# Optimization experiments

Hardware: AMD Instinct MI355X
Metric: run time of the kernel (lower is better)

## Reference

```python
import jax, jax.numpy as jnp
import numpy as np

N, B, T, C = 1024, 4, 12, 64
D, H, K, E = 64, 2, 3, 16384  # out_dim, gat heads, num_kernel, edges per kernel
NEG_SLOPE_ATTN = 0.2   # DGL GATConv default
NEG_SLOPE_ACT = 0.01   # nn.LeakyReLU default


def setup_inputs() -> dict:
    key = jax.random.key(0)
    ks = jax.random.split(key, 12)
    input_feature = jax.random.normal(ks[0], (B, N, T, C), dtype=jnp.float32)
    # edge lists per kernel, with self loops appended (dgl.add_self_loop)
    loops = jnp.broadcast_to(jnp.arange(N, dtype=jnp.int32), (K, N))
    src_idx = jnp.concatenate(
        [jax.random.randint(ks[1], (K, E), 0, N, dtype=jnp.int32), loops], axis=1)
    dst_idx = jnp.concatenate(
        [jax.random.randint(ks[2], (K, E), 0, N, dtype=jnp.int32), loops], axis=1)
    # GATConv params per kernel: fc (no bias), attn_l/attn_r, output bias
    fc_w = jax.random.normal(ks[3], (K, C, H * D), dtype=jnp.float32) * 0.1
    attn_l = jax.random.normal(ks[4], (K, H, D), dtype=jnp.float32) * 0.1
    attn_r = jax.random.normal(ks[5], (K, H, D), dtype=jnp.float32) * 0.1
    gat_bias = jax.random.normal(ks[6], (K, H * D), dtype=jnp.float32) * 0.02
    # per-kernel merge weight, init std 0.05 as in init_weight()
    weight = jax.random.normal(ks[7], (K,), dtype=jnp.float32) * 0.05
    # merge MLP: Linear(H*D -> D)
    merge_w = jax.random.normal(ks[8], (H * D, D), dtype=jnp.float32) * 0.05
    merge_b = jax.random.normal(ks[9], (D,), dtype=jnp.float32) * 0.02
    return {"input_feature": input_feature, "fc_w": fc_w, "attn_l": attn_l,
            "attn_r": attn_r, "gat_bias": gat_bias, "weight": weight,
            "merge_w": merge_w, "merge_b": merge_b,
            "src_idx": src_idx, "dst_idx": dst_idx}


def _gat_conv(x, fc_w, attn_l, attn_r, bias, src, dst):
    """DGL GATConv on feature x: [N,B,T,C] -> [N,B,T,H,D]."""
    feat = jnp.einsum('nbtc,ce->nbte', x, fc_w).reshape(N, B, T, H, D)
    el = jnp.einsum('nbthd,hd->nbth', feat, attn_l)  # [N,B,T,H]
    er = jnp.einsum('nbthd,hd->nbth', feat, attn_r)
    e = jax.nn.leaky_relu(el[src] + er[dst], NEG_SLOPE_ATTN)  # [Etot,B,T,H]
    # segment softmax over destination neighborhoods (self loops guarantee >=1 edge)
    emax = jax.ops.segment_max(e, dst, num_segments=N)
    a = jnp.exp(e - emax[dst])
    denom = jax.ops.segment_sum(a, dst, num_segments=N)
    alpha = a / denom[dst]
    msg = alpha[..., None] * feat[src]  # [Etot,B,T,H,D]
    rst = jax.ops.segment_sum(msg, dst, num_segments=N)
    return rst + bias.reshape(H, D)


def reference(input_feature, fc_w, attn_l, attn_r, gat_bias, weight,
              merge_w, merge_b, src_idx, dst_idx):
    x = jnp.transpose(input_feature, (1, 0, 2, 3))  # [N,B,T,C]
    result = jnp.zeros((N, B, T, H, D), dtype=x.dtype)
    for i in range(K):  # small fixed set of dilated kernels
        result = result + weight[i] * _gat_conv(
            x, fc_w[i], attn_l[i], attn_r[i], gat_bias[i], src_idx[i], dst_idx[i])
    merged = result.reshape(N, B, T, H * D) @ merge_w + merge_b  # [N,B,T,D]
    out = jax.nn.leaky_relu(merged, NEG_SLOPE_ACT) + x  # residual = Identity (C==D)
    return jnp.transpose(out, (1, 0, 2, 3))  # [B,N,T,D]
```

## Files before the change

### kernel.cpp

```cpp
#include <hip/hip_runtime.h>

#define NN   1024
#define TT   12
#define CC   64
#define DD   64
#define HH   2
#define KK   3
#define ETOT 17408
#define BT   48
#define BTH  96
#define HD   128
#define NODES (KK * NN + 1)
#define PADN  (KK * NN)
#define CSR_CAP (KK * ETOT + 12 * NN)
#define LOG2E 1.44269504f
#define MT   128
#define NBLK (NN * BT / MT)
#define EDGE_BLOCKS ((KK * ETOT + 255) / 256)
#define FEAT_BLOCKS (KK * NBLK)
#define BIG_BLOCKS (EDGE_BLOCKS + FEAT_BLOCKS + NN)
#define RUNCAP 208

typedef __attribute__((ext_vector_type(8))) short s8v;
typedef __attribute__((ext_vector_type(4))) float f4v;

__device__ __forceinline__ float bf_lo(unsigned int u) {
    return __uint_as_float(u << 16);
}
__device__ __forceinline__ float bf_hi(unsigned int u) {
    return __uint_as_float(u & 0xFFFF0000u);
}
__device__ __forceinline__ unsigned short f2bf(float f) {
    unsigned int u = __float_as_uint(f);
    u += 0x7FFFu + ((u >> 16) & 1u);
    return (unsigned short)(u >> 16);
}
__device__ __forceinline__ unsigned int pack2(float a, float b) {
    return (unsigned int)f2bf(a) | ((unsigned int)f2bf(b) << 16);
}
__device__ __forceinline__ float rlf(float v, int lane) {
    return __int_as_float(__builtin_amdgcn_readlane(__float_as_int(v), lane));
}

__global__ __launch_bounds__(256) void aux_kernel(
    const int* __restrict__ dst_idx, int* __restrict__ counts,
    const float* __restrict__ fc_w, const float* __restrict__ attn_l,
    const float* __restrict__ attn_r, float* __restrict__ alc, float* __restrict__ arc,
    uint2* __restrict__ featp, float* __restrict__ elp)
{
    int bid = blockIdx.x;
    int t = threadIdx.x;
    if (bid < EDGE_BLOCKS) {
        int tid = bid * 256 + t;
        if (tid < KK * ETOT) {
            int k = tid / ETOT;
            atomicAdd(&counts[k * NN + dst_idx[tid]], 1);
        }
    } else {
        for (int item = t; item < KK * HH * CC; item += 256) {
            int kh = item >> 6, c = item & 63;
            int k = kh >> 1, h = kh & 1;
            float sl = 0.f, sr = 0.f;
            #pragma unroll
            for (int dd = 0; dd < 64; ++dd) {
                float wv = fc_w[k * CC * HD + c * HD + h * 64 + dd];
                sl = fmaf(wv, attn_l[k * HD + h * 64 + dd], sl);
                sr = fmaf(wv, attn_r[k * HD + h * 64 + dd], sr);
            }
            alc[item] = sl * LOG2E;
            arc[item] = sr * LOG2E;
        }
        for (int item = t; item < 24 * 64; item += 256)
            featp[((size_t)(item >> 6) * NODES + PADN) * 64 + (item & 63)] = make_uint2(0u, 0u);
        for (int item = t; item < 24 * 4; item += 256)
            elp[((size_t)(item >> 2) * NODES + PADN) * 4 + (item & 3)] = -1e30f;
    }
}

__global__ __launch_bounds__(1024) void scan_kernel(
    const int* __restrict__ counts,
    int4* __restrict__ segs, int* __restrict__ cursor, int* __restrict__ csr_comb)
{
    int n = threadIdx.x;
    int c0 = counts[n], c1 = counts[NN + n], c2 = counts[2 * NN + n];
    int p0 = (c0 + 3) & ~3, p1 = (c1 + 3) & ~3, p2 = (c2 + 3) & ~3;
    int tot = p0 + p1 + p2;
    __shared__ int buf[NN];
    buf[n] = tot;
    __syncthreads();
    for (int off = 1; off < NN; off <<= 1) {
        int v = (n >= off) ? buf[n - off] : 0;
        __syncthreads();
        buf[n] += v;
        __syncthreads();
    }
    int excl = buf[n] - tot;
    int4 sg;
    sg.x = excl; sg.y = excl + p0; sg.z = excl + p0 + p1; sg.w = excl + tot;
    segs[n] = sg;
    cursor[n] = sg.x;
    cursor[NN + n] = sg.y;
    cursor[2 * NN + n] = sg.z;
    for (int j = sg.x + c0; j < sg.y; ++j) csr_comb[j] = PADN;
    for (int j = sg.y + c1; j < sg.z; ++j) csr_comb[j] = PADN;
    for (int j = sg.z + c2; j < sg.w; ++j) csr_comb[j] = PADN;
}

__global__ __launch_bounds__(256) void big_kernel(
    const int* __restrict__ src_idx, const int* __restrict__ dst_idx,
    int* __restrict__ cursor, int* __restrict__ csr_comb,
    const float* __restrict__ x, const float* __restrict__ fc_w,
    uint2* __restrict__ featp,
    const float* __restrict__ alc, const float* __restrict__ arc,
    float* __restrict__ elp, float* __restrict__ er)
{
    __shared__ __align__(16) char smem[32768];
    int bid = blockIdx.x;
    int t = threadIdx.x;

    if (bid < EDGE_BLOCKS) {
        int tid = bid * 256 + t;
        if (tid < KK * ETOT) {
            int k = tid / ETOT;
            int pos = atomicAdd(&cursor[k * NN + dst_idx[tid]], 1);
            csr_comb[pos] = k * NN + src_idx[tid];
        }
        return;
    }
    if (bid < EDGE_BLOCKS + FEAT_BLOCKS) {
        int kb = bid - EDGE_BLOCKS;
        int k  = kb / NBLK;
        int m0 = (kb - k * NBLK) * MT;
        int w  = t >> 6, l = t & 63;
        unsigned short* As = (unsigned short*)smem;
        unsigned short* Ws = (unsigned short*)(smem + 16384);

        #pragma unroll
        for (int rep = 0; rep < 4; ++rep) {
            int gid = t + 256 * rep;
            int row = gid >> 3, g = gid & 7;
            int m = m0 + row;
            int n = m / BT, bt = m - n * BT;
            int b = bt / TT, tt2 = bt - b * TT;
            const float* xr = &x[(((size_t)b * NN + n) * TT + tt2) * CC + g * 8];
            float4 v0 = *(const float4*)xr;
            float4 v1 = *(const float4*)(xr + 4);
            uint4 pk = { pack2(v0.x, v0.y), pack2(v0.z, v0.w),
                         pack2(v1.x, v1.y), pack2(v1.z, v1.w) };
            *(uint4*)((char*)As + row * 128 + ((g ^ (row & 7)) << 4)) = pk;
        }
        #pragma unroll
        for (int rep = 0; rep < 4; ++rep) {
            int gid = t + 256 * rep;
            int e = gid & 127, g = gid >> 7;
            float v[8];
            #pragma unroll
            for (int jj = 0; jj < 8; ++jj)
                v[jj] = fc_w[(size_t)k * CC * HD + (g * 8 + jj) * HD + e];
            uint4 pk = { pack2(v[0], v[1]), pack2(v[2], v[3]),
                         pack2(v[4], v[5]), pack2(v[6], v[7]) };
            *(uint4*)((char*)Ws + e * 128 + ((g ^ (e & 7)) << 4)) = pk;
        }
        __syncthreads();

        int Mw = (w & 1) * 64;
        int Nw = (w >> 1) * 64;
        int rsel = l & 15, ksel = l >> 4;

        f4v acc[4][4];
        #pragma unroll
        for (int mi = 0; mi < 4; ++mi)
            #pragma unroll
            for (int nf = 0; nf < 4; ++nf)
                acc[mi][nf] = (f4v){0.f, 0.f, 0.f, 0.f};

        s8v af[4][2], bf[4][2];
        #pragma unroll
        for (int mi = 0; mi < 4; ++mi)
            #pragma unroll
            for (int ks = 0; ks < 2; ++ks) {
                int row = Mw + mi * 16 + rsel;
                int g = ks * 4 + ksel;
                af[mi][ks] = *(const s8v*)((const char*)As + row * 128 + ((g ^ (row & 7)) << 4));
            }
        #pragma unroll
        for (int nf = 0; nf < 4; ++nf)
            #pragma unroll
            for (int ks = 0; ks < 2; ++ks) {
                int e = Nw + nf * 16 + rsel;
                int g = ks * 4 + ksel;
                bf[nf][ks] = *(const s8v*)((const char*)Ws + e * 128 + ((g ^ (e & 7)) << 4));
            }

        #pragma unroll
        for (int mi = 0; mi < 4; ++mi)
            #pragma unroll
            for (int nf = 0; nf < 4; ++nf) {
                acc[mi][nf] = __builtin_amdgcn_mfma_f32_16x16x32_bf16(
                    af[mi][0], bf[nf][0], acc[mi][nf], 0, 0, 0);
                acc[mi][nf] = __builtin_amdgcn_mfma_f32_16x16x32_bf16(
                    af[mi][1], bf[nf][1], acc[mi][nf], 0, 0, 0);
            }

        int i0 = (l >> 4) * 4;
        #pragma unroll
        for (int mi = 0; mi < 4; ++mi) {
            int m = m0 + Mw + mi * 16 + i0;
            int n = m / BT, bt = m - n * BT;
            #pragma unroll
            for (int nf = 0; nf < 4; ++nf) {
                int e = Nw + nf * 16 + (l & 15);
                int h = e >> 6, d = e & 63;
                int s = (bt >> 2) * 2 + h;
                uint2 o = { pack2(acc[mi][nf][0], acc[mi][nf][1]),
                            pack2(acc[mi][nf][2], acc[mi][nf][3]) };
                featp[((size_t)s * NODES + k * NN + n) * 64 + d] = o;
            }
        }
        return;
    }

    {
        int n = bid - (EDGE_BLOCKS + FEAT_BLOCKS);
        float* x_lds = (float*)smem;
        float* cl    = (float*)(smem + 12288);
        float* cr    = (float*)(smem + 12288 + 1536);

        for (int i = t; i < BT * CC; i += 256) {
            int bt = i >> 6, c = i & 63;
            int b = bt / TT, tt = bt - b * TT;
            x_lds[i] = x[(((size_t)b * NN + n) * TT + tt) * CC + c];
        }
        for (int i = t; i < KK * HH * CC; i += 256) { cl[i] = alc[i]; cr[i] = arc[i]; }
        __syncthreads();

        if (t < BTH) {
            int hh = t / BT, bt = t - hh * BT;
            #pragma unroll
            for (int k = 0; k < KK; ++k) {
                const float* alp = &cl[(k * HH + hh) * CC];
                const float* arp = &cr[(k * HH + hh) * CC];
                float sl = 0.f, sr = 0.f;
                #pragma unroll
                for (int cc = 0; cc < CC; ++cc) {
                    int c = (cc + bt) & 63;
                    float xv = x_lds[bt * CC + c];
                    sl = fmaf(xv, alp[c], sl);
                    sr = fmaf(xv, arp[c], sr);
                }
                int s = (bt >> 2) * 2 + hh;
                elp[((size_t)s * NODES + k * NN + n) * 4 + (bt & 3)] = sl;
                er[((size_t)(k * NN + n)) * BTH + t] = sr;
            }
        }
    }
}

#define EDGE_FMA8(F, A)                                        \
    r0 = fmaf((A).x, bf_lo((F).x), r0);                        \
    r1 = fmaf((A).y, bf_hi((F).x), r1);                        \
    r2 = fmaf((A).z, bf_lo((F).y), r2);                        \
    r3 = fmaf((A).w, bf_hi((F).y), r3);

#define PHASE1(JB, JE, KIDX, SC4) {                                            \
    int jb = (JB), je = (JE);                                                  \
    float erv = er[((size_t)((KIDX) * NN + n)) * BTH + h * BT + btg4 * 4 + bt];\
    float ss = 0.f;                                                            \
    for (int j0 = jb; j0 < je; j0 += 16) {                                     \
        int jj = j0 + joff;                                                    \
        float a = 0.f;                                                         \
        if (jj < je) {                                                         \
            int idx = csr_comb[jj];                                            \
            float ev = ep[idx * 4 + bt] + erv;                                 \
            ev = fmaxf(ev, ev * 0.2f);                                         \
            a = __builtin_amdgcn_exp2f(ev);                                    \
            alds[w][jj - base0][bt] = a;                                       \
        }                                                                      \
        ss += a;                                                               \
    }                                                                          \
    _Pragma("unroll")                                                          \
    for (int off = 4; off < 64; off <<= 1) ss += __shfl_xor(ss, off, 64);      \
    float wk_ = weight[KIDX];                                                  \
    SC4 = make_float4(wk_ * __builtin_amdgcn_rcpf(rlf(ss, 0)),                 \
                      wk_ * __builtin_amdgcn_rcpf(rlf(ss, 1)),                 \
                      wk_ * __builtin_amdgcn_rcpf(rlf(ss, 2)),                 \
                      wk_ * __builtin_amdgcn_rcpf(rlf(ss, 3))); }

#define PHASE2(JB, JE, SC4) {                                                  \
    int jb = __builtin_amdgcn_readfirstlane(JB);                               \
    int je = __builtin_amdgcn_readfirstlane(JE);                               \
    float r0 = 0.f, r1 = 0.f, r2 = 0.f, r3 = 0.f;                              \
    int jj = jb;                                                               \
    for (; jj + 8 <= je; jj += 8) {                                            \
        int4 ia = *(const int4*)&csr_comb[jj];                                 \
        int4 ib = *(const int4*)&csr_comb[jj + 4];                             \
        int i0 = __builtin_amdgcn_readfirstlane(ia.x);                         \
        int i1 = __builtin_amdgcn_readfirstlane(ia.y);                         \
        int i2 = __builtin_amdgcn_readfirstlane(ia.z);                         \
        int i3 = __builtin_amdgcn_readfirstlane(ia.w);                         \
        int i4 = __builtin_amdgcn_readfirstlane(ib.x);                         \
        int i5 = __builtin_amdgcn_readfirstlane(ib.y);                         \
        int i6 = __builtin_amdgcn_readfirstlane(ib.z);                         \
        int i7 = __builtin_amdgcn_readfirstlane(ib.w);                         \
        uint2 f0 = fb[(size_t)i0 * 64];                                        \
        uint2 f1 = fb[(size_t)i1 * 64];                                        \
        uint2 f2 = fb[(size_t)i2 * 64];                                        \
        uint2 f3 = fb[(size_t)i3 * 64];                                        \
        uint2 f4 = fb[(size_t)i4 * 64];                                        \
        uint2 f5 = fb[(size_t)i5 * 64];                                        \
        uint2 f6 = fb[(size_t)i6 * 64];                                        \
        uint2 f7 = fb[(size_t)i7 * 64];                                        \
        float4 A0 = *(const float4*)&alds[w][jj - base0 + 0][0];               \
        float4 A1 = *(const float4*)&alds[w][jj - base0 + 1][0];               \
        float4 A2 = *(const float4*)&alds[w][jj - base0 + 2][0];               \
        float4 A3 = *(const float4*)&alds[w][jj - base0 + 3][0];               \
        float4 A4 = *(const float4*)&alds[w][jj - base0 + 4][0];               \
        float4 A5 = *(const float4*)&alds[w][jj - base0 + 5][0];               \
        float4 A6 = *(const float4*)&alds[w][jj - base0 + 6][0];               \
        float4 A7 = *(const float4*)&alds[w][jj - base0 + 7][0];               \
        EDGE_FMA8(f0, A0); EDGE_FMA8(f1, A1);                                  \
        EDGE_FMA8(f2, A2); EDGE_FMA8(f3, A3);                                  \
        EDGE_FMA8(f4, A4); EDGE_FMA8(f5, A5);                                  \
        EDGE_FMA8(f6, A6); EDGE_FMA8(f7, A7);                                  \
    }                                                                          \
    if (jj < je) {                                                             \
        int4 ia = *(const int4*)&csr_comb[jj];                                 \
        int i0 = __builtin_amdgcn_readfirstlane(ia.x);                         \
        int i1 = __builtin_amdgcn_readfirstlane(ia.y);                         \
        int i2 = __builtin_amdgcn_readfirstlane(ia.z);                         \
        int i3 = __builtin_amdgcn_readfirstlane(ia.w);                         \
        uint2 f0 = fb[(size_t)i0 * 64];                                        \
        uint2 f1 = fb[(size_t)i1 * 64];                                        \
        uint2 f2 = fb[(size_t)i2 * 64];                                        \
        uint2 f3 = fb[(size_t)i3 * 64];                                        \
        float4 A0 = *(const float4*)&alds[w][jj - base0 + 0][0];               \
        float4 A1 = *(const float4*)&alds[w][jj - base0 + 1][0];               \
        float4 A2 = *(const float4*)&alds[w][jj - base0 + 2][0];               \
        float4 A3 = *(const float4*)&alds[w][jj - base0 + 3][0];               \
        EDGE_FMA8(f0, A0); EDGE_FMA8(f1, A1);                                  \
        EDGE_FMA8(f2, A2); EDGE_FMA8(f3, A3);                                  \
    }                                                                          \
    acc0 = fmaf(r0, (SC4).x, acc0); acc1 = fmaf(r1, (SC4).y, acc1);            \
    acc2 = fmaf(r2, (SC4).z, acc2); acc3 = fmaf(r3, (SC4).w, acc3); }

__global__ __launch_bounds__(256) void agg_kernel(
    const uint2* __restrict__ featp,
    const float* __restrict__ elp,
    const float* __restrict__ er,
    const int4* __restrict__ segs, const int* __restrict__ csr_comb,
    const float* __restrict__ gat_bias, const float* __restrict__ weight,
    unsigned short* __restrict__ gatb)
{
    int j = ((int)blockIdx.x >> 3) + 768 * ((int)blockIdx.x & 7);
    int s = j >> 8;
    int g = j & 255;
    int w = threadIdx.x >> 6;
    int l = threadIdx.x & 63;
    int n = g * 4 + w;
    int btg4 = s >> 1, h = s & 1;
    int e = h * 64 + l;

    __shared__ __align__(16) float alds[4][RUNCAP][4];

    const uint2* fb = featp + (size_t)s * NODES * 64 + l;
    const float* ep = elp + (size_t)s * NODES * 4;
    int4 sg = segs[n];
    int base0 = __builtin_amdgcn_readfirstlane(sg.x);

    int joff = l >> 2, bt = l & 3;
    float4 sc0, sc1, sc2;
    PHASE1(sg.x, sg.y, 0, sc0)
    PHASE1(sg.y, sg.z, 1, sc1)
    PHASE1(sg.z, sg.w, 2, sc2)

    float acc0 = 0.f, acc1 = 0.f, acc2 = 0.f, acc3 = 0.f;
    PHASE2(sg.x, sg.y, sc0)
    PHASE2(sg.y, sg.z, sc1)
    PHASE2(sg.z, sg.w, sc2)

    float wb = weight[0] * gat_bias[e] + weight[1] * gat_bias[HD + e]
             + weight[2] * gat_bias[2 * HD + e];
    acc0 += wb; acc1 += wb; acc2 += wb; acc3 += wb;

    size_t row = (size_t)n * BT + btg4 * 4;
    gatb[(row + 0) * HD + e] = f2bf(acc0);
    gatb[(row + 1) * HD + e] = f2bf(acc1);
    gatb[(row + 2) * HD + e] = f2bf(acc2);
    gatb[(row + 3) * HD + e] = f2bf(acc3);
}
#undef EDGE_FMA8
#undef PHASE1
#undef PHASE2

__global__ __launch_bounds__(256) void merge_mfma_kernel(
    const unsigned short* __restrict__ gatb,
    const float* __restrict__ merge_w, const float* __restrict__ merge_b,
    const float* __restrict__ x, float* __restrict__ out)
{
    int m0 = blockIdx.x * 128;
    int t = threadIdx.x, w = t >> 6, l = t & 63;

    __shared__ __align__(16) unsigned short As[128 * 128];
    __shared__ __align__(16) unsigned short Bs[64 * 128];

    #pragma unroll
    for (int rep = 0; rep < 8; ++rep) {
        int gid = t + 256 * rep;
        int row = gid >> 4, gg = gid & 15;
        uint4 v = *(const uint4*)((const char*)gatb + ((size_t)(m0 + row)) * 256 + gg * 16);
        *(uint4*)((char*)As + row * 256 + ((gg ^ (row & 15)) << 4)) = v;
    }
    #pragma unroll
    for (int rep = 0; rep < 4; ++rep) {
        int gid = t + 256 * rep;
        int col = gid >> 4, gg = gid & 15;
        float v[8];
        #pragma unroll
        for (int jj = 0; jj < 8; ++jj)
            v[jj] = merge_w[(gg * 8 + jj) * DD + col];
        uint4 pk = { pack2(v[0], v[1]), pack2(v[2], v[3]),
                     pack2(v[4], v[5]), pack2(v[6], v[7]) };
        *(uint4*)((char*)Bs + col * 256 + ((gg ^ (col & 15)) << 4)) = pk;
    }
    __syncthreads();

    int Mw = (w & 1) * 64, Nw = (w >> 1) * 32;
    int rsel = l & 15, ksel = l >> 4;

    f4v acc[4][2];
    #pragma unroll
    for (int mi = 0; mi < 4; ++mi)
        #pragma unroll
        for (int nf = 0; nf < 2; ++nf)
            acc[mi][nf] = (f4v){0.f, 0.f, 0.f, 0.f};

    s8v af[4][4], bfr[2][4];
    #pragma unroll
    for (int mi = 0; mi < 4; ++mi)
        #pragma unroll
        for (int ks = 0; ks < 4; ++ks) {
            int row = Mw + mi * 16 + rsel;
            int g2 = ks * 4 + ksel;
            af[mi][ks] = *(const s8v*)((const char*)As + row * 256 + ((g2 ^ (row & 15)) << 4));
        }
    #pragma unroll
    for (int nf = 0; nf < 2; ++nf)
        #pragma unroll
        for (int ks = 0; ks < 4; ++ks) {
            int col = Nw + nf * 16 + rsel;
            int g2 = ks * 4 + ksel;
            bfr[nf][ks] = *(const s8v*)((const char*)Bs + col * 256 + ((g2 ^ (col & 15)) << 4));
        }

    #pragma unroll
    for (int mi = 0; mi < 4; ++mi)
        #pragma unroll
        for (int nf = 0; nf < 2; ++nf)
            #pragma unroll
            for (int ks = 0; ks < 4; ++ks)
                acc[mi][nf] = __builtin_amdgcn_mfma_f32_16x16x32_bf16(
                    af[mi][ks], bfr[nf][ks], acc[mi][nf], 0, 0, 0);

    int i0 = (l >> 4) * 4;
    #pragma unroll
    for (int mi = 0; mi < 4; ++mi) {
        int m = m0 + Mw + mi * 16 + i0;
        int n = m / BT, btb = m - n * BT;
        int b = btb / TT, t0 = btb - b * TT;
        #pragma unroll
        for (int nf = 0; nf < 2; ++nf) {
            int dd = Nw + nf * 16 + (l & 15);
            float mb = merge_b[dd];
            #pragma unroll
            for (int reg = 0; reg < 4; ++reg) {
                float mg = acc[mi][nf][reg] + mb;
                mg = mg > 0.f ? mg : mg * 0.01f;
                size_t oidx = (((size_t)b * NN + n) * TT + t0 + reg) * DD + dd;
                out[oidx] = mg + x[oidx];
            }
        }
    }
}

extern "C" void kernel_launch(void* const* d_in, const int* in_sizes, int n_in,
                              void* d_out, int out_size, void* d_ws, size_t ws_size,
                              hipStream_t stream)
{
    const float* x        = (const float*)d_in[0];
    const float* fc_w     = (const float*)d_in[1];
    const float* attn_l   = (const float*)d_in[2];
    const float* attn_r   = (const float*)d_in[3];
    const float* gat_bias = (const float*)d_in[4];
    const float* weight   = (const float*)d_in[5];
    const float* merge_w  = (const float*)d_in[6];
    const float* merge_b  = (const float*)d_in[7];
    const int*   src_idx  = (const int*)d_in[8];
    const int*   dst_idx  = (const int*)d_in[9];
    float*       out      = (float*)d_out;

    char* p = (char*)d_ws;
    auto carve = [&](size_t bytes) { char* r = p; p += (bytes + 15) & ~size_t(15); return r; };
    uint2* featp   = (uint2*)carve(sizeof(uint2) * (size_t)24 * NODES * 64);
    unsigned short* gatb = (unsigned short*)carve(sizeof(unsigned short) * (size_t)NN * BT * HD);
    float* elp     = (float*)carve(sizeof(float) * (size_t)24 * NODES * 4);
    float* er      = (float*)carve(sizeof(float) * (size_t)KK * NN * BTH);
    float* alc     = (float*)carve(sizeof(float) * KK * HH * CC);
    float* arc     = (float*)carve(sizeof(float) * KK * HH * CC);
    int*   counts  = (int*)carve(sizeof(int) * KK * NN);
    int*   cursor  = (int*)carve(sizeof(int) * KK * NN);
    int4*  segs    = (int4*)carve(sizeof(int4) * NN);
    int*   csr_comb= (int*)carve(sizeof(int) * (CSR_CAP + 80));

    hipMemsetAsync(counts, 0, sizeof(int) * KK * NN, stream);

    aux_kernel<<<EDGE_BLOCKS + 1, 256, 0, stream>>>(
        dst_idx, counts, fc_w, attn_l, attn_r, alc, arc, featp, elp);

    scan_kernel<<<1, 1024, 0, stream>>>(counts, segs, cursor, csr_comb);

    big_kernel<<<BIG_BLOCKS, 256, 0, stream>>>(
        src_idx, dst_idx, cursor, csr_comb, x, fc_w, featp, alc, arc, elp, er);

    agg_kernel<<<24 * 256, 256, 0, stream>>>(
        featp, elp, er, segs, csr_comb, gat_bias, weight, gatb);

    merge_mfma_kernel<<<NN * BT / 128, 256, 0, stream>>>(gatb, merge_w, merge_b, x, out);
}
```

Measured before the change: 145.4 us.

## Widen feature slices to 8 bt per lane and interleave softmax/aggregate phases

Changes the packed feature layout from 24 slices of 4 bt values (uint2) to 12 slices of 8 bt values (uint4). The MFMA epilogue now pairs lanes with a shuffle so each writer stores one 16-byte chunk. The aggregation kernel processes 8 bt per lane, which halves the block count and the number of index loads and gathers per edge. It also runs each kernel's softmax phase right before its aggregation instead of all three first, so the LDS alpha buffer can be shorter (RUNCAP 144). The trade-offs are more registers per thread, fewer resident blocks, and a smaller per-segment cap on the LDS run buffer.

Measured after the change: 134.3 us. -7.6%, faster.

```diff
diff --git a/kernel.cpp b/kernel.cpp
--- a/kernel.cpp
+++ b/kernel.cpp
@@ -19,7 +19,8 @@
 #define EDGE_BLOCKS ((KK * ETOT + 255) / 256)
 #define FEAT_BLOCKS (KK * NBLK)
 #define BIG_BLOCKS (EDGE_BLOCKS + FEAT_BLOCKS + NN)
-#define RUNCAP 208
+#define NSL  12
+#define RUNCAP 144
 
 typedef __attribute__((ext_vector_type(8))) short s8v;
 typedef __attribute__((ext_vector_type(4))) float f4v;
@@ -46,7 +47,7 @@
     const int* __restrict__ dst_idx, int* __restrict__ counts,
     const float* __restrict__ fc_w, const float* __restrict__ attn_l,
     const float* __restrict__ attn_r, float* __restrict__ alc, float* __restrict__ arc,
-    uint2* __restrict__ featp, float* __restrict__ elp)
+    uint4* __restrict__ featp, float* __restrict__ elp)
 {
     int bid = blockIdx.x;
     int t = threadIdx.x;
@@ -70,10 +71,11 @@
             alc[item] = sl * LOG2E;
             arc[item] = sr * LOG2E;
         }
-        for (int item = t; item < 24 * 64; item += 256)
-            featp[((size_t)(item >> 6) * NODES + PADN) * 64 + (item & 63)] = make_uint2(0u, 0u);
-        for (int item = t; item < 24 * 4; item += 256)
-            elp[((size_t)(item >> 2) * NODES + PADN) * 4 + (item & 3)] = -1e30f;
+        for (int item = t; item < NSL * 64; item += 256)
+            featp[((size_t)(item >> 6) * NODES + PADN) * 64 + (item & 63)] =
+                make_uint4(0u, 0u, 0u, 0u);
+        for (int item = t; item < NSL * 8; item += 256)
+            elp[((size_t)(item >> 3) * NODES + PADN) * 8 + (item & 7)] = -1e30f;
     }
 }
 
@@ -110,7 +112,7 @@
     const int* __restrict__ src_idx, const int* __restrict__ dst_idx,
     int* __restrict__ cursor, int* __restrict__ csr_comb,
     const float* __restrict__ x, const float* __restrict__ fc_w,
-    uint2* __restrict__ featp,
+    uint4* __restrict__ featp,
     const float* __restrict__ alc, const float* __restrict__ arc,
     float* __restrict__ elp, float* __restrict__ er)
 {
@@ -203,18 +205,24 @@
             }
 
         int i0 = (l >> 4) * 4;
+        bool writer = ((l >> 4) & 1) == 0;
         #pragma unroll
         for (int mi = 0; mi < 4; ++mi) {
             int m = m0 + Mw + mi * 16 + i0;
             int n = m / BT, bt = m - n * BT;
             #pragma unroll
             for (int nf = 0; nf < 4; ++nf) {
-                int e = Nw + nf * 16 + (l & 15);
-                int h = e >> 6, d = e & 63;
-                int s = (bt >> 2) * 2 + h;
                 uint2 o = { pack2(acc[mi][nf][0], acc[mi][nf][1]),
                             pack2(acc[mi][nf][2], acc[mi][nf][3]) };
-                featp[((size_t)s * NODES + k * NN + n) * 64 + d] = o;
+                unsigned int px = (unsigned int)__shfl_xor((int)o.x, 16, 64);
+                unsigned int py = (unsigned int)__shfl_xor((int)o.y, 16, 64);
+                if (writer) {
+                    int e = Nw + nf * 16 + (l & 15);
+                    int h = e >> 6, d = e & 63;
+                    int s = ((bt >> 3) << 1) + h;
+                    featp[((size_t)s * NODES + k * NN + n) * 64 + d] =
+                        make_uint4(o.x, o.y, px, py);
+                }
             }
         }
         return;
@@ -248,147 +256,136 @@
                     sl = fmaf(xv, alp[c], sl);
                     sr = fmaf(xv, arp[c], sr);
                 }
-                int s = (bt >> 2) * 2 + hh;
-                elp[((size_t)s * NODES + k * NN + n) * 4 + (bt & 3)] = sl;
+                int s = ((bt >> 3) << 1) + hh;
+                elp[((size_t)s * NODES + k * NN + n) * 8 + (bt & 7)] = sl;
                 er[((size_t)(k * NN + n)) * BTH + t] = sr;
             }
         }
     }
 }
 
-#define EDGE_FMA8(F, A)                                        \
-    r0 = fmaf((A).x, bf_lo((F).x), r0);                        \
-    r1 = fmaf((A).y, bf_hi((F).x), r1);                        \
-    r2 = fmaf((A).z, bf_lo((F).y), r2);                        \
-    r3 = fmaf((A).w, bf_hi((F).y), r3);
-
-#define PHASE1(JB, JE, KIDX, SC4) {                                            \
+#define EFMA(F, LO, HI)                                        \
+    r0 = fmaf((LO).x, bf_lo((F).x), r0);                       \
+    r1 = fmaf((LO).y, bf_hi((F).x), r1);                       \
+    r2 = fmaf((LO).z, bf_lo((F).y), r2);                       \
+    r3 = fmaf((LO).w, bf_hi((F).y), r3);                       \
+    r4 = fmaf((HI).x, bf_lo((F).z), r4);                       \
+    r5 = fmaf((HI).y, bf_hi((F).z), r5);                       \
+    r6 = fmaf((HI).z, bf_lo((F).w), r6);                       \
+    r7 = fmaf((HI).w, bf_hi((F).w), r7);
+
+#define PHASE1(JB, JE, KIDX, SCLO, SCHI) {                                     \
     int jb = (JB), je = (JE);                                                  \
-    float erv = er[((size_t)((KIDX) * NN + n)) * BTH + h * BT + btg4 * 4 + bt];\
+    float erv = er[((size_t)((KIDX) * NN + n)) * BTH + h * BT + btg8 * 8 + btq];\
     float ss = 0.f;                                                            \
-    for (int j0 = jb; j0 < je; j0 += 16) {                                     \
+    for (int j0 = jb; j0 < je; j0 += 8) {                                      \
         int jj = j0 + joff;                                                    \
         float a = 0.f;                                                         \
         if (jj < je) {                                                         \
             int idx = csr_comb[jj];                                            \
-            float ev = ep[idx * 4 + bt] + erv;                                 \
+            float ev = elp[(size_t)sbase8 + (size_t)idx * 8 + btq] + erv;      \
             ev = fmaxf(ev, ev * 0.2f);                                         \
             a = __builtin_amdgcn_exp2f(ev);                                    \
-            alds[w][jj - base0][bt] = a;                                       \
+            alds[w][jj - base0][btq] = a;                                      \
         }                                                                      \
         ss += a;                                                               \
     }                                                                          \
-    _Pragma("unroll")                                                          \
-    for (int off = 4; off < 64; off <<= 1) ss += __shfl_xor(ss, off, 64);      \
+    ss += __shfl_xor(ss, 8, 64);                                               \
+    ss += __shfl_xor(ss, 16, 64);                                              \
+    ss += __shfl_xor(ss, 32, 64);                                              \
     float wk_ = weight[KIDX];                                                  \
-    SC4 = make_float4(wk_ * __builtin_amdgcn_rcpf(rlf(ss, 0)),                 \
-                      wk_ * __builtin_amdgcn_rcpf(rlf(ss, 1)),                 \
-                      wk_ * __builtin_amdgcn_rcpf(rlf(ss, 2)),                 \
-                      wk_ * __builtin_amdgcn_rcpf(rlf(ss, 3))); }
-
-#define PHASE2(JB, JE, SC4) {                                                  \
+    SCLO = make_float4(wk_ * __builtin_amdgcn_rcpf(rlf(ss, 0)),                \
+                       wk_ * __builtin_amdgcn_rcpf(rlf(ss, 1)),                \
+                       wk_ * __builtin_amdgcn_rcpf(rlf(ss, 2)),                \
+                       wk_ * __builtin_amdgcn_rcpf(rlf(ss, 3)));               \
+    SCHI = make_float4(wk_ * __builtin_amdgcn_rcpf(rlf(ss, 4)),                \
+                       wk_ * __builtin_amdgcn_rcpf(rlf(ss, 5)),                \
+                       wk_ * __builtin_amdgcn_rcpf(rlf(ss, 6)),                \
+                       wk_ * __builtin_amdgcn_rcpf(rlf(ss, 7))); }
+
+#define PHASE2(JB, JE, SCLO, SCHI) {                                           \
     int jb = __builtin_amdgcn_readfirstlane(JB);                               \
     int je = __builtin_amdgcn_readfirstlane(JE);                               \
-    float r0 = 0.f, r1 = 0.f, r2 = 0.f, r3 = 0.f;                              \
-    int jj = jb;                                                               \
-    for (; jj + 8 <= je; jj += 8) {                                            \
-        int4 ia = *(const int4*)&csr_comb[jj];                                 \
-        int4 ib = *(const int4*)&csr_comb[jj + 4];                             \
-        int i0 = __builtin_amdgcn_readfirstlane(ia.x);                         \
-        int i1 = __builtin_amdgcn_readfirstlane(ia.y);                         \
-        int i2 = __builtin_amdgcn_readfirstlane(ia.z);                         \
-        int i3 = __builtin_amdgcn_readfirstlane(ia.w);                         \
-        int i4 = __builtin_amdgcn_readfirstlane(ib.x);                         \
-        int i5 = __builtin_amdgcn_readfirstlane(ib.y);                         \
-        int i6 = __builtin_amdgcn_readfirstlane(ib.z);                         \
-        int i7 = __builtin_amdgcn_readfirstlane(ib.w);                         \
-        uint2 f0 = fb[(size_t)i0 * 64];                                        \
-        uint2 f1 = fb[(size_t)i1 * 64];                                        \
-        uint2 f2 = fb[(size_t)i2 * 64];                                        \
-        uint2 f3 = fb[(size_t)i3 * 64];                                        \
-        uint2 f4 = fb[(size_t)i4 * 64];                                        \
-        uint2 f5 = fb[(size_t)i5 * 64];                                        \
-        uint2 f6 = fb[(size_t)i6 * 64];                                        \
-        uint2 f7 = fb[(size_t)i7 * 64];                                        \
-        float4 A0 = *(const float4*)&alds[w][jj - base0 + 0][0];               \
-        float4 A1 = *(const float4*)&alds[w][jj - base0 + 1][0];               \
-        float4 A2 = *(const float4*)&alds[w][jj - base0 + 2][0];               \
-        float4 A3 = *(const float4*)&alds[w][jj - base0 + 3][0];               \
-        float4 A4 = *(const float4*)&alds[w][jj - base0 + 4][0];               \
-        float4 A5 = *(const float4*)&alds[w][jj - base0 + 5][0];               \
-        float4 A6 = *(const float4*)&alds[w][jj - base0 + 6][0];               \
-        float4 A7 = *(const float4*)&alds[w][jj - base0 + 7][0];               \
-        EDGE_FMA8(f0, A0); EDGE_FMA8(f1, A1);                                  \
-        EDGE_FMA8(f2, A2); EDGE_FMA8(f3, A3);                                  \
-        EDGE_FMA8(f4, A4); EDGE_FMA8(f5, A5);                                  \
-        EDGE_FMA8(f6, A6); EDGE_FMA8(f7, A7);                                  \
+    float r0=0.f,r1=0.f,r2=0.f,r3=0.f,r4=0.f,r5=0.f,r6=0.f,r7=0.f;             \
+    for (int jj = jb; jj < je; jj += 4) {                                      \
+        int4 i4 = *(const int4*)&csr_comb[jj];                                 \
+        int i0 = __builtin_amdgcn_readfirstlane(i4.x);                         \
+        int i1 = __builtin_amdgcn_readfirstlane(i4.y);                         \
+        int i2 = __builtin_amdgcn_readfirstlane(i4.z);                         \
+        int i3 = __builtin_amdgcn_readfirstlane(i4.w);                         \
+        uint4 f0 = fb[(size_t)i0 * 64];                                        \
+        uint4 f1 = fb[(size_t)i1 * 64];                                        \
+        uint4 f2 = fb[(size_t)i2 * 64];                                        \
+        uint4 f3 = fb[(size_t)i3 * 64];                                        \
+        float4 L0 = *(const float4*)&alds[w][jj - base0 + 0][0];               \
+        float4 H0 = *(const float4*)&alds[w][jj - base0 + 0][4];               \
+        float4 L1 = *(const float4*)&alds[w][jj - base0 + 1][0];               \
+        float4 H1 = *(const float4*)&alds[w][jj - base0 + 1][4];               \
+        float4 L2 = *(const float4*)&alds[w][jj - base0 + 2][0];               \
+        float4 H2 = *(const float4*)&alds[w][jj - base0 + 2][4];               \
+        float4 L3 = *(const float4*)&alds[w][jj - base0 + 3][0];               \
+        float4 H3 = *(const float4*)&alds[w][jj - base0 + 3][4];               \
+        EFMA(f0, L0, H0); EFMA(f1, L1, H1);                                    \
+        EFMA(f2, L2, H2); EFMA(f3, L3, H3);                                    \
     }                                                                          \
-    if (jj < je) {                                                             \
-        int4 ia = *(const int4*)&csr_comb[jj];                                 \
-        int i0 = __builtin_amdgcn_readfirstlane(ia.x);                         \
-        int i1 = __builtin_amdgcn_readfirstlane(ia.y);                         \
-        int i2 = __builtin_amdgcn_readfirstlane(ia.z);                         \
-        int i3 = __builtin_amdgcn_readfirstlane(ia.w);                         \
-        uint2 f0 = fb[(size_t)i0 * 64];                                        \
-        uint2 f1 = fb[(size_t)i1 * 64];                                        \
-        uint2 f2 = fb[(size_t)i2 * 64];                                        \
-        uint2 f3 = fb[(size_t)i3 * 64];                                        \
-        float4 A0 = *(const float4*)&alds[w][jj - base0 + 0][0];               \
-        float4 A1 = *(const float4*)&alds[w][jj - base0 + 1][0];               \
-        float4 A2 = *(const float4*)&alds[w][jj - base0 + 2][0];               \
-        float4 A3 = *(const float4*)&alds[w][jj - base0 + 3][0];               \
-        EDGE_FMA8(f0, A0); EDGE_FMA8(f1, A1);                                  \
-        EDGE_FMA8(f2, A2); EDGE_FMA8(f3, A3);                                  \
-    }                                                                          \
-    acc0 = fmaf(r0, (SC4).x, acc0); acc1 = fmaf(r1, (SC4).y, acc1);            \
-    acc2 = fmaf(r2, (SC4).z, acc2); acc3 = fmaf(r3, (SC4).w, acc3); }
+    acc0 = fmaf(r0, (SCLO).x, acc0); acc1 = fmaf(r1, (SCLO).y, acc1);          \
+    acc2 = fmaf(r2, (SCLO).z, acc2); acc3 = fmaf(r3, (SCLO).w, acc3);          \
+    acc4 = fmaf(r4, (SCHI).x, acc4); acc5 = fmaf(r5, (SCHI).y, acc5);          \
+    acc6 = fmaf(r6, (SCHI).z, acc6); acc7 = fmaf(r7, (SCHI).w, acc7); }
 
 __global__ __launch_bounds__(256) void agg_kernel(
-    const uint2* __restrict__ featp,
+    const uint4* __restrict__ featp,
     const float* __restrict__ elp,
     const float* __restrict__ er,
     const int4* __restrict__ segs, const int* __restrict__ csr_comb,
     const float* __restrict__ gat_bias, const float* __restrict__ weight,
     unsigned short* __restrict__ gatb)
 {
-    int j = ((int)blockIdx.x >> 3) + 768 * ((int)blockIdx.x & 7);
-    int s = j >> 8;
-    int g = j & 255;
+    int xcd = (int)blockIdx.x & 7;
+    int q   = (int)blockIdx.x >> 3;
+    int j   = q + 384 * xcd;
+    int s   = j >> 8;
+    int g   = j & 255;
     int w = threadIdx.x >> 6;
     int l = threadIdx.x & 63;
     int n = g * 4 + w;
-    int btg4 = s >> 1, h = s & 1;
+    int btg8 = s >> 1, h = s & 1;
     int e = h * 64 + l;
 
-    __shared__ __align__(16) float alds[4][RUNCAP][4];
-
-    const uint2* fb = featp + (size_t)s * NODES * 64 + l;
-    const float* ep = elp + (size_t)s * NODES * 4;
+    __shared__ __align__(16) float alds[4][RUNCAP][8];
+
+    const uint4* fb = featp + (size_t)s * NODES * 64 + l;
+    size_t sbase8 = (size_t)s * NODES * 8;
     int4 sg = segs[n];
     int base0 = __builtin_amdgcn_readfirstlane(sg.x);
 
-    int joff = l >> 2, bt = l & 3;
-    float4 sc0, sc1, sc2;
-    PHASE1(sg.x, sg.y, 0, sc0)
-    PHASE1(sg.y, sg.z, 1, sc1)
-    PHASE1(sg.z, sg.w, 2, sc2)
-
-    float acc0 = 0.f, acc1 = 0.f, acc2 = 0.f, acc3 = 0.f;
-    PHASE2(sg.x, sg.y, sc0)
-    PHASE2(sg.y, sg.z, sc1)
-    PHASE2(sg.z, sg.w, sc2)
+    int joff = l >> 3, btq = l & 7;
+    float acc0=0.f,acc1=0.f,acc2=0.f,acc3=0.f,acc4=0.f,acc5=0.f,acc6=0.f,acc7=0.f;
+    float4 sclo, schi;
+
+    PHASE1(sg.x, sg.y, 0, sclo, schi)
+    PHASE2(sg.x, sg.y, sclo, schi)
+    PHASE1(sg.y, sg.z, 1, sclo, schi)
+    PHASE2(sg.y, sg.z, sclo, schi)
+    PHASE1(sg.z, sg.w, 2, sclo, schi)
+    PHASE2(sg.z, sg.w, sclo, schi)
 
     float wb = weight[0] * gat_bias[e] + weight[1] * gat_bias[HD + e]
              + weight[2] * gat_bias[2 * HD + e];
     acc0 += wb; acc1 += wb; acc2 += wb; acc3 += wb;
-
-    size_t row = (size_t)n * BT + btg4 * 4;
+    acc4 += wb; acc5 += wb; acc6 += wb; acc7 += wb;
+
+    size_t row = (size_t)n * BT + btg8 * 8;
     gatb[(row + 0) * HD + e] = f2bf(acc0);
     gatb[(row + 1) * HD + e] = f2bf(acc1);
     gatb[(row + 2) * HD + e] = f2bf(acc2);
     gatb[(row + 3) * HD + e] = f2bf(acc3);
-}
-#undef EDGE_FMA8
+    gatb[(row + 4) * HD + e] = f2bf(acc4);
+    gatb[(row + 5) * HD + e] = f2bf(acc5);
+    gatb[(row + 6) * HD + e] = f2bf(acc6);
+    gatb[(row + 7) * HD + e] = f2bf(acc7);
+}
+#undef EFMA
 #undef PHASE1
 #undef PHASE2
 
@@ -500,9 +497,9 @@
 
     char* p = (char*)d_ws;
     auto carve = [&](size_t bytes) { char* r = p; p += (bytes + 15) & ~size_t(15); return r; };
-    uint2* featp   = (uint2*)carve(sizeof(uint2) * (size_t)24 * NODES * 64);
+    uint4* featp   = (uint4*)carve(sizeof(uint4) * (size_t)NSL * NODES * 64);
     unsigned short* gatb = (unsigned short*)carve(sizeof(unsigned short) * (size_t)NN * BT * HD);
-    float* elp     = (float*)carve(sizeof(float) * (size_t)24 * NODES * 4);
+    float* elp     = (float*)carve(sizeof(float) * (size_t)NSL * NODES * 8);
     float* er      = (float*)carve(sizeof(float) * (size_t)KK * NN * BTH);
     float* alc     = (float*)carve(sizeof(float) * KK * HH * CC);
     float* arc     = (float*)carve(sizeof(float) * KK * HH * CC);
@@ -521,7 +518,7 @@
     big_kernel<<<BIG_BLOCKS, 256, 0, stream>>>(
         src_idx, dst_idx, cursor, csr_comb, x, fc_w, featp, alc, arc, elp, er);
 
-    agg_kernel<<<24 * 256, 256, 0, stream>>>(
+    agg_kernel<<<NSL * 256, 256, 0, stream>>>(
         featp, elp, er, segs, csr_comb, gat_bias, weight, gatb);
 
     merge_mfma_kernel<<<NN * BT / 128, 256, 0, stream>>>(gatb, merge_w, merge_b, x, out);
```
